# Optimization experiments

Measured on AMD Instinct MI355X. Metric: run time of the kernel, lower is better.

## Reference

```python
import jax, jax.numpy as jnp
import numpy as np

B, NQ, NK, DIM, H = 2, 2048, 4096, 256, 8
HD = DIM // H  # head dim = 32


def setup_inputs() -> dict:
    key = jax.random.key(0)
    ks = jax.random.split(key, 8)
    s = 0.02  # init scale for weights
    return {
        "xq": jax.random.normal(ks[0], (B, NQ, DIM), jnp.float32),
        "xk": jax.random.normal(ks[1], (B, NK, DIM), jnp.float32),
        "xv": jax.random.normal(ks[2], (B, NK, DIM), jnp.float32),
        # torch nn.Linear weights: shape (out, in), y = x @ W.T + b
        "wq": jax.random.normal(ks[3], (DIM, DIM), jnp.float32) * s,
        "wk": jax.random.normal(ks[4], (DIM, DIM), jnp.float32) * s,
        "wv": jax.random.normal(ks[5], (DIM, DIM), jnp.float32) * s,
        "wp": jax.random.normal(ks[6], (DIM, DIM), jnp.float32) * s,
        "bp": jnp.zeros((DIM,), jnp.float32),
    }


def reference(xq, xk, xv, wq, wk, wv, wp, bp):
    scale = HD ** (-0.5)
    Bq, Nq, C = xq.shape
    Nk = xk.shape[1]
    # project and split heads: [B, H, N, HD]
    q = jnp.einsum('bnc,dc->bnd', xq, wq).reshape(Bq, Nq, H, HD).transpose(0, 2, 1, 3)
    k = jnp.einsum('bnc,dc->bnd', xk, wk).reshape(Bq, Nk, H, HD).transpose(0, 2, 1, 3)
    v = jnp.einsum('bnc,dc->bnd', xv, wv).reshape(Bq, Nk, H, HD).transpose(0, 2, 1, 3)
    # pre-softmax scores [B, H, Nq, Nk]
    attn = jnp.einsum('bhqd,bhkd->bhqk', q, k) * scale
    attn_save = attn.sum(axis=1) / H  # head-mean of pre-softmax scores
    p = jax.nn.softmax(attn, axis=-1)
    x = jnp.einsum('bhqk,bhkd->bhqd', p, v).transpose(0, 2, 1, 3).reshape(Bq, Nq, C)
    x = jnp.einsum('bnc,dc->bnd', x, wp) + bp
    return x, attn_save
```

## Files before the change

### kernel.cpp

```cpp
#include <hip/hip_runtime.h>

typedef unsigned int u32;
typedef unsigned short u16;
typedef short bf16x8 __attribute__((ext_vector_type(8)));
typedef float f32x4 __attribute__((ext_vector_type(4)));
typedef float f32x16 __attribute__((ext_vector_type(16)));
typedef int i32x4 __attribute__((ext_vector_type(4)));
typedef __bf16 bf16x2 __attribute__((ext_vector_type(2)));
typedef float f32x2 __attribute__((ext_vector_type(2)));

#define KSPLIT 4

__device__ __forceinline__ u32 pack2bf(float a, float b) {
    u32 ua = __float_as_uint(a), ub = __float_as_uint(b);
    ua = (ua + 0x7fffu + ((ua >> 16) & 1u)) >> 16;
    ub = (ub + 0x7fffu + ((ub >> 16) & 1u)) >> 16;
    return (ua & 0xffffu) | (ub << 16);
}
__device__ __forceinline__ u16 bf1(float a) {
    u32 ua = __float_as_uint(a);
    return (u16)((ua + 0x7fffu + ((ua >> 16) & 1u)) >> 16);
}
__device__ __forceinline__ u32 b2(float a, float b) {
    f32x2 f; f[0] = a; f[1] = b;
    bf16x2 h = __builtin_convertvector(f, bf16x2);
    return __builtin_bit_cast(u32, h);
}

__global__ __launch_bounds__(256) void cvt_w4(const float* __restrict__ wq,
                                              const float* __restrict__ wk,
                                              const float* __restrict__ wv,
                                              const float* __restrict__ wp,
                                              u16* __restrict__ dst) {
    int i = blockIdx.x * 256 + threadIdx.x;
    int which = i >> 14;
    int j = i & 16383;
    const float* s = which == 0 ? wq : which == 1 ? wk : which == 2 ? wv : wp;
    float4 a = ((const float4*)s)[j];
    uint2 v;
    v.x = pack2bf(a.x, a.y);
    v.y = pack2bf(a.z, a.w);
    ((uint2*)(dst + which * 65536))[j] = v;
}

__global__ __launch_bounds__(256) void proj_all(const float* __restrict__ xq,
                                                const float* __restrict__ xk,
                                                const float* __restrict__ xv,
                                                const u16* __restrict__ W4,
                                                u16* __restrict__ Qb,
                                                u16* __restrict__ K2,
                                                u16* __restrict__ V2,
                                                float qalpha) {
    int bx = blockIdx.x;
    int mode = bx < 64 ? 0 : (bx < 192 ? 1 : 2);
    int xb = mode == 0 ? bx : (mode == 1 ? bx - 64 : bx - 192);
    const float* X = mode == 0 ? xq : mode == 1 ? xk : xv;
    const u16* Wb = W4 + mode * 65536;

    __shared__ u16 xs[64 * 256];
    int t = threadIdx.x;
    int m0 = xb * 64;
#pragma unroll
    for (int i = 0; i < 8; i++) {
        int c16 = t + 256 * i;
        int row = c16 >> 5, col16 = c16 & 31;
        const float4* src = (const float4*)(X + (size_t)(m0 + row) * 256 + col16 * 8);
        float4 a = src[0], b2v = src[1];
        uint4 v;
        v.x = pack2bf(a.x, a.y); v.y = pack2bf(a.z, a.w);
        v.z = pack2bf(b2v.x, b2v.y); v.w = pack2bf(b2v.z, b2v.w);
        int byteoff = row * 512 + ((col16 * 16) ^ ((row & 7) << 4));
        *(uint4*)((char*)xs + byteoff) = v;
    }
    __syncthreads();
    int lane = t & 63, w = t >> 6;
    int lq = lane & 15, g = lane >> 4;
    int rowA = w * 16 + lq;
    f32x4 acc[16];
    f32x4 z = {0.f, 0.f, 0.f, 0.f};
#pragma unroll
    for (int nt = 0; nt < 16; nt++) acc[nt] = z;
#pragma unroll
    for (int kk = 0; kk < 8; kk++) {
        bf16x8 aF = *(const bf16x8*)((const char*)xs + rowA * 512 +
                                     ((kk * 64 + g * 16) ^ ((rowA & 7) << 4)));
#pragma unroll
        for (int nt = 0; nt < 16; nt++) {
            bf16x8 bF = *(const bf16x8*)(Wb + (size_t)(nt * 16 + lq) * 256 + kk * 32 + g * 8);
            acc[nt] = __builtin_amdgcn_mfma_f32_16x16x32_bf16(aF, bF, acc[nt], 0, 0, 0);
        }
    }
    if (mode == 0) {
#pragma unroll
        for (int nt = 0; nt < 16; nt++) {
            int col = nt * 16 + lq;
#pragma unroll
            for (int r = 0; r < 4; r++) {
                int m = m0 + w * 16 + g * 4 + r;
                Qb[(size_t)m * 256 + col] = bf1(acc[nt][r] * qalpha);
            }
        }
    } else if (mode == 1) {
        int m = m0 + w * 16 + g * 4;
        int b = m >> 12, n = m & 4095;
#pragma unroll
        for (int nt = 0; nt < 16; nt++) {
            int d = nt * 16 + lq;
            int h = d >> 5, d32 = d & 31;
            u16* p = K2 + ((size_t)(b * 8 + h) * 4096 + n) * 32 + d32;
#pragma unroll
            for (int r = 0; r < 4; r++) p[r * 32] = bf1(acc[nt][r]);
        }
    } else {
        int m = m0 + w * 16 + g * 4;
        int b = m >> 12, n = m & 4095;
        int s = n >> 5;
        int t5 = n & 31;
        int pklo = (t5 & 19) | ((t5 << 1) & 8) | ((t5 >> 1) & 4);
#pragma unroll
        for (int nt = 0; nt < 16; nt++) {
            int d = nt * 16 + lq;
            int h = d >> 5, d32 = d & 31;
            uint2 v;
            v.x = pack2bf(acc[nt][0], acc[nt][1]);
            v.y = pack2bf(acc[nt][2], acc[nt][3]);
            *(uint2*)(V2 + ((((size_t)(b * 8 + h) * 128 + s) * 32 + d32) * 32 + pklo)) = v;
        }
    }
}

__global__ __launch_bounds__(256) void save_gemm(const u16* __restrict__ Qb,
                                                 const u16* __restrict__ K2,
                                                 float* __restrict__ sv) {
    const float SAVE = 0.125f * 0.69314718055994530942f;
    int b = blockIdx.z;
    int m0 = blockIdx.y * 128, n0 = blockIdx.x * 128;
    int t = threadIdx.x, lane = t & 63, wv = t >> 6;
    int wr = wv >> 1, wc = wv & 1;
    int lq = lane & 15, g = lane >> 4;
    const u16* Q = Qb + (size_t)b * 2048 * 256;
    f32x4 acc[4][4];
    f32x4 z = {0.f, 0.f, 0.f, 0.f};
#pragma unroll
    for (int mt = 0; mt < 4; mt++)
#pragma unroll
        for (int nt = 0; nt < 4; nt++) acc[mt][nt] = z;
#pragma unroll
    for (int kk = 0; kk < 8; kk++) {
        bf16x8 aF[4], bF[4];
#pragma unroll
        for (int mt = 0; mt < 4; mt++)
            aF[mt] = *(const bf16x8*)(Q + (size_t)(m0 + wr * 64 + mt * 16 + lq) * 256 + kk * 32 + g * 8);
#pragma unroll
        for (int nt = 0; nt < 4; nt++)
            bF[nt] = *(const bf16x8*)(K2 + ((size_t)(b * 8 + kk) * 4096 + n0 + wc * 64 + nt * 16 + lq) * 32 + g * 8);
#pragma unroll
        for (int mt = 0; mt < 4; mt++)
#pragma unroll
            for (int nt = 0; nt < 4; nt++)
                acc[mt][nt] = __builtin_amdgcn_mfma_f32_16x16x32_bf16(aF[mt], bF[nt], acc[mt][nt], 0, 0, 0);
    }
#pragma unroll
    for (int mt = 0; mt < 4; mt++) {
#pragma unroll
        for (int nt = 0; nt < 4; nt++) {
            int col = n0 + wc * 64 + nt * 16 + lq;
#pragma unroll
            for (int r = 0; r < 4; r++) {
                int row = m0 + wr * 64 + mt * 16 + g * 4 + r;
                sv[((size_t)b * 2048 + row) * 4096 + col] = acc[mt][nt][r] * SAVE;
            }
        }
    }
}

__global__ __launch_bounds__(256, 2) void attn_part(const u16* __restrict__ Qb,
                                                    const u16* __restrict__ K2,
                                                    const u16* __restrict__ V2,
                                                    float* __restrict__ PO,
                                                    float* __restrict__ PL) {
    int id = blockIdx.x;
    int h = id & 7;
    int r0 = id >> 3;
    int qblk = r0 & 7;
    int b = (r0 >> 3) & 1;
    int part = r0 >> 4;
    int bh = b * 8 + h;
    int t = threadIdx.x, lane = t & 63, w = t >> 6;
    int lq = lane & 31, hl = lane >> 5;
    int qa = qblk * 256 + w * 64 + lq;
    const u16* Qrow = Qb + ((size_t)(b * 2048 + qa)) * 256 + h * 32 + hl * 8;
    bf16x8 qf00 = *(const bf16x8*)(Qrow);
    bf16x8 qf01 = *(const bf16x8*)(Qrow + 16);
    bf16x8 qf10 = *(const bf16x8*)(Qrow + 32 * 256);
    bf16x8 qf11 = *(const bf16x8*)(Qrow + 32 * 256 + 16);
    const u16* Kh = K2 + ((size_t)bh * 4096 + part * 1024 + lq) * 32 + hl * 8;
    const u16* Vh = V2 + (size_t)bh * 131072 + part * 32768 + lq * 32 + hl * 8;
    f32x16 z16 = {};
    f32x16 o0 = z16, o1 = z16;
    float l0 = 0.f, l1 = 0.f;
    for (int it = 0; it < 16; ++it) {
#pragma unroll
        for (int s = 0; s < 2; s++) {
            const u16* kp = Kh + (it * 64 + s * 32) * 32;
            bf16x8 kf0 = *(const bf16x8*)(kp);
            bf16x8 kf1 = *(const bf16x8*)(kp + 16);
            const u16* vp = Vh + (it * 2 + s) * 1024;
            bf16x8 vf0 = *(const bf16x8*)(vp);
            bf16x8 vf1 = *(const bf16x8*)(vp + 16);
            f32x16 sA = __builtin_amdgcn_mfma_f32_32x32x16_bf16(kf0, qf00, z16, 0, 0, 0);
            sA = __builtin_amdgcn_mfma_f32_32x32x16_bf16(kf1, qf01, sA, 0, 0, 0);
            f32x16 sB = __builtin_amdgcn_mfma_f32_32x32x16_bf16(kf0, qf10, z16, 0, 0, 0);
            sB = __builtin_amdgcn_mfma_f32_32x32x16_bf16(kf1, qf11, sB, 0, 0, 0);
            float pA[16], pB[16];
#pragma unroll
            for (int k = 0; k < 16; k++) pA[k] = __builtin_amdgcn_exp2f(sA[k]);
#pragma unroll
            for (int k = 0; k < 16; k++) pB[k] = __builtin_amdgcn_exp2f(sB[k]);
            float la = 0.f, lb = 0.f;
#pragma unroll
            for (int k = 0; k < 16; k++) { la += pA[k]; lb += pB[k]; }
            l0 += la; l1 += lb;
            i32x4 wa0, wa1, wb0, wb1;
#pragma unroll
            for (int j = 0; j < 4; j++) {
                wa0[j] = (int)b2(pA[2 * j], pA[2 * j + 1]);
                wa1[j] = (int)b2(pA[8 + 2 * j], pA[9 + 2 * j]);
                wb0[j] = (int)b2(pB[2 * j], pB[2 * j + 1]);
                wb1[j] = (int)b2(pB[8 + 2 * j], pB[9 + 2 * j]);
            }
            bf16x8 pa0 = __builtin_bit_cast(bf16x8, wa0);
            bf16x8 pa1 = __builtin_bit_cast(bf16x8, wa1);
            bf16x8 pb0 = __builtin_bit_cast(bf16x8, wb0);
            bf16x8 pb1 = __builtin_bit_cast(bf16x8, wb1);
            o0 = __builtin_amdgcn_mfma_f32_32x32x16_bf16(vf0, pa0, o0, 0, 0, 0);
            o0 = __builtin_amdgcn_mfma_f32_32x32x16_bf16(vf1, pa1, o0, 0, 0, 0);
            o1 = __builtin_amdgcn_mfma_f32_32x32x16_bf16(vf0, pb0, o1, 0, 0, 0);
            o1 = __builtin_amdgcn_mfma_f32_32x32x16_bf16(vf1, pb1, o1, 0, 0, 0);
        }
    }
    l0 += __shfl_xor(l0, 32);
    l1 += __shfl_xor(l1, 32);
    size_t rowa = (size_t)(part * 16 + bh) * 2048 + qa;
    float* poa = PO + rowa * 32;
    float* pob = PO + (rowa + 32) * 32;
#pragma unroll
    for (int cc = 0; cc < 4; cc++) {
        f32x4 va, vb;
#pragma unroll
        for (int i = 0; i < 4; i++) { va[i] = o0[4 * cc + i]; vb[i] = o1[4 * cc + i]; }
        *(f32x4*)(poa + cc * 8 + hl * 4) = va;
        *(f32x4*)(pob + cc * 8 + hl * 4) = vb;
    }
    if (hl == 0) {
        PL[rowa] = l0;
        PL[rowa + 32] = l1;
    }
}

__global__ __launch_bounds__(256) void attn_combine(const float* __restrict__ PO,
                                                    const float* __restrict__ PL,
                                                    u16* __restrict__ Ob) {
    int idx = blockIdx.x * 256 + threadIdx.x;
    int bh = idx >> 11, q = idx & 2047;
    f32x4 acc[8];
    f32x4 z = {0.f, 0.f, 0.f, 0.f};
#pragma unroll
    for (int j = 0; j < 8; j++) acc[j] = z;
    float L = 0.f;
#pragma unroll
    for (int p = 0; p < KSPLIT; p++) {
        int i = ((p * 16 + bh) << 11) + q;
        L += PL[i];
        const f32x4* src = (const f32x4*)(PO + ((size_t)i * 32));
#pragma unroll
        for (int j = 0; j < 8; j++) acc[j] += src[j];
    }
    float inv = 1.0f / L;
    u16* dst = Ob + ((size_t)((bh >> 3) * 2048 + q)) * 256 + (bh & 7) * 32;
    u32 words[16];
#pragma unroll
    for (int j = 0; j < 8; j++) {
        words[2 * j] = pack2bf(acc[j][0] * inv, acc[j][1] * inv);
        words[2 * j + 1] = pack2bf(acc[j][2] * inv, acc[j][3] * inv);
    }
#pragma unroll
    for (int v = 0; v < 4; v++) {
        uint4 t4;
        t4.x = words[4 * v]; t4.y = words[4 * v + 1]; t4.z = words[4 * v + 2]; t4.w = words[4 * v + 3];
        *(uint4*)(dst + v * 8) = t4;
    }
}

__global__ __launch_bounds__(64) void oproj(const u16* __restrict__ Ob,
                                            const u16* __restrict__ Wp,
                                            const float* __restrict__ bp,
                                            float* __restrict__ out) {
    int t = threadIdx.x, lq = t & 15, g = t >> 4;
    int m0 = blockIdx.x * 16;
    int nb = blockIdx.y * 4;
    f32x4 acc[4];
    f32x4 z = {0.f, 0.f, 0.f, 0.f};
#pragma unroll
    for (int j = 0; j < 4; j++) acc[j] = z;
#pragma unroll
    for (int kk = 0; kk < 8; kk++) {
        bf16x8 aF = *(const bf16x8*)(Ob + (size_t)(m0 + lq) * 256 + kk * 32 + g * 8);
#pragma unroll
        for (int j = 0; j < 4; j++) {
            bf16x8 bF = *(const bf16x8*)(Wp + (size_t)((nb + j) * 16 + lq) * 256 + kk * 32 + g * 8);
            acc[j] = __builtin_amdgcn_mfma_f32_16x16x32_bf16(aF, bF, acc[j], 0, 0, 0);
        }
    }
#pragma unroll
    for (int j = 0; j < 4; j++) {
        int col = (nb + j) * 16 + lq;
        float bias = bp[col];
#pragma unroll
        for (int r = 0; r < 4; r++) {
            int row = m0 + g * 4 + r;
            out[(size_t)row * 256 + col] = acc[j][r] + bias;
        }
    }
}

extern "C" void kernel_launch(void* const* d_in, const int* in_sizes, int n_in,
                              void* d_out, int out_size, void* d_ws, size_t ws_size,
                              hipStream_t stream) {
    const float* xq = (const float*)d_in[0];
    const float* xk = (const float*)d_in[1];
    const float* xv = (const float*)d_in[2];
    const float* wq = (const float*)d_in[3];
    const float* wk = (const float*)d_in[4];
    const float* wv = (const float*)d_in[5];
    const float* wp = (const float*)d_in[6];
    const float* bp = (const float*)d_in[7];
    float* out = (float*)d_out;

    u16* wsb = (u16*)d_ws;
    u16* W4 = wsb;
    u16* WPb = wsb + 196608;
    u16* Qb = wsb + 262144;
    u16* K2 = Qb + 1048576;
    u16* V2 = K2 + 2097152;
    u16* Ob = V2 + 2097152;

    float* outw = out + 1048576;
    float* PO = outw;
    float* PL = PO + 4194304;

    const float qalpha = 0.17677669529663687f * 1.4426950408889634f;

    cvt_w4<<<256, 256, 0, stream>>>(wq, wk, wv, wp, W4);
    proj_all<<<320, 256, 0, stream>>>(xq, xk, xv, W4, Qb, K2, V2, qalpha);

    attn_part<<<512, 256, 0, stream>>>(Qb, K2, V2, PO, PL);
    attn_combine<<<128, 256, 0, stream>>>(PO, PL, Ob);
    oproj<<<dim3(256, 4), 64, 0, stream>>>(Ob, WPb, bp, out);

    save_gemm<<<dim3(32, 16, 2), 256, 0, stream>>>(Qb, K2, out + 1048576);
}
```

Before: 116.7 us.

## Double key split in attention and fuse split combine with output projection

```diff
diff --git a/kernel.cpp b/kernel.cpp
--- a/kernel.cpp
+++ b/kernel.cpp
@@ -9,7 +9,7 @@
 typedef __bf16 bf16x2 __attribute__((ext_vector_type(2)));
 typedef float f32x2 __attribute__((ext_vector_type(2)));
 
-#define KSPLIT 4
+#define KSPLIT 8
 
 __device__ __forceinline__ u32 pack2bf(float a, float b) {
     u32 ua = __float_as_uint(a), ub = __float_as_uint(b);
@@ -174,7 +174,7 @@
     }
 }
 
-__global__ __launch_bounds__(256, 2) void attn_part(const u16* __restrict__ Qb,
+__global__ __launch_bounds__(256, 4) void attn_part(const u16* __restrict__ Qb,
                                                     const u16* __restrict__ K2,
                                                     const u16* __restrict__ V2,
                                                     float* __restrict__ PO,
@@ -194,12 +194,12 @@
     bf16x8 qf01 = *(const bf16x8*)(Qrow + 16);
     bf16x8 qf10 = *(const bf16x8*)(Qrow + 32 * 256);
     bf16x8 qf11 = *(const bf16x8*)(Qrow + 32 * 256 + 16);
-    const u16* Kh = K2 + ((size_t)bh * 4096 + part * 1024 + lq) * 32 + hl * 8;
-    const u16* Vh = V2 + (size_t)bh * 131072 + part * 32768 + lq * 32 + hl * 8;
+    const u16* Kh = K2 + ((size_t)bh * 4096 + part * 512 + lq) * 32 + hl * 8;
+    const u16* Vh = V2 + (size_t)bh * 131072 + part * 16384 + lq * 32 + hl * 8;
     f32x16 z16 = {};
     f32x16 o0 = z16, o1 = z16;
     float l0 = 0.f, l1 = 0.f;
-    for (int it = 0; it < 16; ++it) {
+    for (int it = 0; it < 8; ++it) {
 #pragma unroll
         for (int s = 0; s < 2; s++) {
             const u16* kp = Kh + (it * 64 + s * 32) * 32;
@@ -258,68 +258,72 @@
     }
 }
 
-__global__ __launch_bounds__(256) void attn_combine(const float* __restrict__ PO,
-                                                    const float* __restrict__ PL,
-                                                    u16* __restrict__ Ob) {
-    int idx = blockIdx.x * 256 + threadIdx.x;
-    int bh = idx >> 11, q = idx & 2047;
-    f32x4 acc[8];
+__global__ __launch_bounds__(256) void combine_oproj(const float* __restrict__ PO,
+                                                     const float* __restrict__ PL,
+                                                     const u16* __restrict__ Wp,
+                                                     const float* __restrict__ bp,
+                                                     float* __restrict__ out) {
+    __shared__ u16 os[16 * 256];
+    int t = threadIdx.x;
+    int qloc = t >> 4, chunk = t & 15;
+    int R = blockIdx.x * 16 + qloc;
+    int b = R >> 11, q = R & 2047;
+    int h = chunk >> 1;
+    int d0 = chunk * 16;
+    int d32 = d0 & 31;
+    int bh = b * 8 + h;
+    float acc[16];
+#pragma unroll
+    for (int j = 0; j < 16; j++) acc[j] = 0.f;
+    float L = 0.f;
+#pragma unroll
+    for (int p = 0; p < KSPLIT; p++) {
+        size_t i = ((size_t)(p * 16 + bh) << 11) + q;
+        L += PL[i];
+        const f32x4* src = (const f32x4*)(PO + i * 32 + d32);
+#pragma unroll
+        for (int v = 0; v < 4; v++) {
+            f32x4 x = src[v];
+#pragma unroll
+            for (int e = 0; e < 4; e++) acc[4 * v + e] += x[e];
+        }
+    }
+    float inv = 1.0f / L;
+    uint4 w0, w1;
+    w0.x = b2(acc[0] * inv, acc[1] * inv);   w0.y = b2(acc[2] * inv, acc[3] * inv);
+    w0.z = b2(acc[4] * inv, acc[5] * inv);   w0.w = b2(acc[6] * inv, acc[7] * inv);
+    w1.x = b2(acc[8] * inv, acc[9] * inv);   w1.y = b2(acc[10] * inv, acc[11] * inv);
+    w1.z = b2(acc[12] * inv, acc[13] * inv); w1.w = b2(acc[14] * inv, acc[15] * inv);
+    int col16a = d0 >> 3;
+    *(uint4*)((char*)os + qloc * 512 + ((col16a * 16) ^ ((qloc & 7) << 4))) = w0;
+    *(uint4*)((char*)os + qloc * 512 + (((col16a + 1) * 16) ^ ((qloc & 7) << 4))) = w1;
+    __syncthreads();
+    int lane = t & 63, w = t >> 6;
+    int lq = lane & 15, g = lane >> 4;
+    int nb = w * 4;
+    f32x4 acc4[4];
     f32x4 z = {0.f, 0.f, 0.f, 0.f};
 #pragma unroll
-    for (int j = 0; j < 8; j++) acc[j] = z;
-    float L = 0.f;
-#pragma unroll
-    for (int p = 0; p < KSPLIT; p++) {
-        int i = ((p * 16 + bh) << 11) + q;
-        L += PL[i];
-        const f32x4* src = (const f32x4*)(PO + ((size_t)i * 32));
-#pragma unroll
-        for (int j = 0; j < 8; j++) acc[j] += src[j];
-    }
-    float inv = 1.0f / L;
-    u16* dst = Ob + ((size_t)((bh >> 3) * 2048 + q)) * 256 + (bh & 7) * 32;
-    u32 words[16];
-#pragma unroll
-    for (int j = 0; j < 8; j++) {
-        words[2 * j] = pack2bf(acc[j][0] * inv, acc[j][1] * inv);
-        words[2 * j + 1] = pack2bf(acc[j][2] * inv, acc[j][3] * inv);
-    }
-#pragma unroll
-    for (int v = 0; v < 4; v++) {
-        uint4 t4;
-        t4.x = words[4 * v]; t4.y = words[4 * v + 1]; t4.z = words[4 * v + 2]; t4.w = words[4 * v + 3];
-        *(uint4*)(dst + v * 8) = t4;
-    }
-}
-
-__global__ __launch_bounds__(64) void oproj(const u16* __restrict__ Ob,
-                                            const u16* __restrict__ Wp,
-                                            const float* __restrict__ bp,
-                                            float* __restrict__ out) {
-    int t = threadIdx.x, lq = t & 15, g = t >> 4;
-    int m0 = blockIdx.x * 16;
-    int nb = blockIdx.y * 4;
-    f32x4 acc[4];
-    f32x4 z = {0.f, 0.f, 0.f, 0.f};
-#pragma unroll
-    for (int j = 0; j < 4; j++) acc[j] = z;
+    for (int j = 0; j < 4; j++) acc4[j] = z;
 #pragma unroll
     for (int kk = 0; kk < 8; kk++) {
-        bf16x8 aF = *(const bf16x8*)(Ob + (size_t)(m0 + lq) * 256 + kk * 32 + g * 8);
+        bf16x8 aF = *(const bf16x8*)((const char*)os + lq * 512 +
+                                     ((kk * 64 + g * 16) ^ ((lq & 7) << 4)));
 #pragma unroll
         for (int j = 0; j < 4; j++) {
             bf16x8 bF = *(const bf16x8*)(Wp + (size_t)((nb + j) * 16 + lq) * 256 + kk * 32 + g * 8);
-            acc[j] = __builtin_amdgcn_mfma_f32_16x16x32_bf16(aF, bF, acc[j], 0, 0, 0);
-        }
-    }
+            acc4[j] = __builtin_amdgcn_mfma_f32_16x16x32_bf16(aF, bF, acc4[j], 0, 0, 0);
+        }
+    }
+    int R0 = blockIdx.x * 16;
 #pragma unroll
     for (int j = 0; j < 4; j++) {
         int col = (nb + j) * 16 + lq;
         float bias = bp[col];
 #pragma unroll
         for (int r = 0; r < 4; r++) {
-            int row = m0 + g * 4 + r;
-            out[(size_t)row * 256 + col] = acc[j][r] + bias;
+            int row = R0 + g * 4 + r;
+            out[(size_t)row * 256 + col] = acc4[j][r] + bias;
         }
     }
 }
@@ -343,20 +347,18 @@
     u16* Qb = wsb + 262144;
     u16* K2 = Qb + 1048576;
     u16* V2 = K2 + 2097152;
-    u16* Ob = V2 + 2097152;
 
     float* outw = out + 1048576;
     float* PO = outw;
-    float* PL = PO + 4194304;
+    float* PL = PO + 8388608;
 
     const float qalpha = 0.17677669529663687f * 1.4426950408889634f;
 
     cvt_w4<<<256, 256, 0, stream>>>(wq, wk, wv, wp, W4);
     proj_all<<<320, 256, 0, stream>>>(xq, xk, xv, W4, Qb, K2, V2, qalpha);
 
-    attn_part<<<512, 256, 0, stream>>>(Qb, K2, V2, PO, PL);
-    attn_combine<<<128, 256, 0, stream>>>(PO, PL, Ob);
-    oproj<<<dim3(256, 4), 64, 0, stream>>>(Ob, WPb, bp, out);
+    attn_part<<<1024, 256, 0, stream>>>(Qb, K2, V2, PO, PL);
+    combine_oproj<<<256, 256, 0, stream>>>(PO, PL, WPb, bp, out);
 
     save_gemm<<<dim3(32, 16, 2), 256, 0, stream>>>(Qb, K2, out + 1048576);
 }
```

Result: slower. 129.3 us (+10.8%).
